# Kernel optimization log

Hardware: AMD Instinct MI355X
Metric: run time of the kernel (lower is better)

Reference implementation:

```python
import jax, jax.numpy as jnp
import numpy as np

B, S, D = 4, 4096, 1024
DFF = 4 * D
ACTIVE = 1024  # ceil(S * 0.25)


def setup_inputs() -> dict:
    key = jax.random.key(0)
    ks = jax.random.split(key, 4)
    x = jax.random.normal(ks[0], (B, S, D), dtype=jnp.float32)
    rw = jax.random.normal(ks[1], (D,), dtype=jnp.float32) * 0.02
    rb = jnp.zeros((1,), dtype=jnp.float32)
    w1 = jax.random.normal(ks[2], (D, DFF), dtype=jnp.float32) * 0.02
    b1 = jnp.zeros((DFF,), dtype=jnp.float32)
    w2 = jax.random.normal(ks[3], (DFF, D), dtype=jnp.float32) * 0.02
    b2 = jnp.zeros((D,), dtype=jnp.float32)
    return {"x": x, "rw": rw, "rb": rb, "w1": w1, "b1": b1,
            "w2": w2, "b2": b2, "active_tokens": ACTIVE}


def reference(x, rw, rb, w1, b1, w2, b2, active_tokens):
    b, s, d = x.shape
    # router: Linear(n_embd, 1) -> [B, S] scores
    scores = jnp.einsum('bsd,d->bs', x, rw) + rb[0]
    # top-k tokens per batch row
    _, idx = jax.lax.top_k(scores, active_tokens)          # [B, K] int32
    sel = jnp.take_along_axis(x, idx[..., None], axis=1)   # [B, K, D]
    # dense MLP on selected tokens (exact GELU as in torch nn.GELU)
    h = jax.nn.gelu(jnp.einsum('bkd,df->bkf', sel, w1) + b1, approximate=False)
    out = jnp.einsum('bkf,fd->bkd', h, w2) + b2            # [B, K, D]
    # sigmoid gate from router scores of selected tokens
    gates = jax.nn.sigmoid(jnp.take_along_axis(scores, idx, axis=1))  # [B, K]
    out = out * gates[..., None]
    # scatter back into zeros at selected positions
    flat_idx = (idx + jnp.arange(b, dtype=idx.dtype)[:, None] * s).reshape(-1)
    flat_out = jnp.zeros((b * s, d), dtype=out.dtype)
    flat_out = flat_out.at[flat_idx].set(out.reshape(-1, d))
    return flat_out.reshape(b, s, d)
```

## Files before the change

### kernel.cpp

```cpp
#include <hip/hip_runtime.h>
#include <hip/hip_bf16.h>
#include <cstdint>
#include <cstddef>

#define Bz 4
#define Sz 4096
#define Dz 1024
#define DFFz 4096
#define KACT 1024

typedef __bf16 bf16;
typedef __attribute__((ext_vector_type(8))) __bf16 bf16x8;
typedef __attribute__((ext_vector_type(4))) __bf16 bf16x4;
typedef __attribute__((ext_vector_type(4))) float f32x4;

__device__ __forceinline__ void async16(const void* g, void* l) {
  __builtin_amdgcn_global_load_lds(
      (const __attribute__((address_space(1))) void*)g,
      (__attribute__((address_space(3))) void*)l, 16, 0, 0);
}

__global__ void router_k(const float* __restrict__ x, const float* __restrict__ rw,
                         const float* __restrict__ rb, float* __restrict__ scores,
                         float4* __restrict__ out4) {
  int row = blockIdx.x * 4 + (threadIdx.x >> 6);
  int lane = threadIdx.x & 63;
  const float4* xr = (const float4*)(x + (size_t)row * Dz);
  const float4* wr = (const float4*)rw;
  float acc = 0.f;
#pragma unroll
  for (int i = 0; i < 4; ++i) {
    float4 a = xr[lane + i * 64];
    float4 w = wr[lane + i * 64];
    acc += a.x * w.x + a.y * w.y + a.z * w.z + a.w * w.w;
  }
#pragma unroll
  for (int d = 32; d; d >>= 1) acc += __shfl_down(acc, d, 64);
  if (lane == 0) scores[row] = acc + rb[0];
  float4* o = out4 + (size_t)blockIdx.x * 4 * (Dz / 4);
  const float4 z = make_float4(0.f, 0.f, 0.f, 0.f);
#pragma unroll
  for (int i = 0; i < 4; ++i) o[threadIdx.x + i * 256] = z;
}

__global__ void transpose_cvt(const float* __restrict__ in, bf16* __restrict__ out,
                              int R, int C) {
  __shared__ float t[32][33];
  int c0 = blockIdx.x * 32, r0 = blockIdx.y * 32;
  int tx = threadIdx.x, ty = threadIdx.y;
#pragma unroll
  for (int i = 0; i < 32; i += 8) t[ty + i][tx] = in[(size_t)(r0 + ty + i) * C + c0 + tx];
  __syncthreads();
#pragma unroll
  for (int i = 0; i < 32; i += 8)
    out[(size_t)(c0 + ty + i) * R + r0 + tx] = (bf16)t[tx][ty + i];
}

__global__ __launch_bounds__(256) void select_gather_k(
    const float* __restrict__ x, const float* __restrict__ scores,
    int* __restrict__ sel_idx, float* __restrict__ gates, bf16* __restrict__ Xsel) {
  int b = blockIdx.x >> 8;
  int s0 = (blockIdx.x & 255) * 16;
  __shared__ float sc[Sz];
  __shared__ int red[16][4];
  __shared__ int rk[16];
  const int tid = threadIdx.x;
  const int wave = tid >> 6, lane = tid & 63;
  const float* srow = scores + (size_t)b * Sz;
#pragma unroll
  for (int i = 0; i < 4; ++i)
    ((float4*)sc)[tid + i * 256] = ((const float4*)srow)[tid + i * 256];
  __syncthreads();
  float mine[16];
#pragma unroll
  for (int j = 0; j < 16; ++j) mine[j] = sc[s0 + j];
  int cnt[16] = {};
  for (int t = tid; t < Sz; t += 256) {
    float o = sc[t];
#pragma unroll
    for (int j = 0; j < 16; ++j)
      cnt[j] += (o > mine[j]) || (o == mine[j] && t < s0 + j);
  }
#pragma unroll
  for (int j = 0; j < 16; ++j) {
    int c = cnt[j];
#pragma unroll
    for (int d = 32; d; d >>= 1) c += __shfl_down(c, d, 64);
    if (lane == 0) red[j][wave] = c;
  }
  __syncthreads();
  if (tid < 16) {
    int rank = red[tid][0] + red[tid][1] + red[tid][2] + red[tid][3];
    rk[tid] = rank;
    if (rank < KACT) {
      int m = b * KACT + rank;
      sel_idx[m] = s0 + tid;
      gates[m] = 1.f / (1.f + expf(-sc[s0 + tid]));
    }
  }
  __syncthreads();
#pragma unroll
  for (int j = 0; j < 16; ++j) {
    int rank = rk[j];
    if (rank >= KACT) continue;
    int m = b * KACT + rank;
    float4 v = ((const float4*)(x + ((size_t)b * Sz + s0 + j) * Dz))[tid];
    bf16x4 o = {(bf16)v.x, (bf16)v.y, (bf16)v.z, (bf16)v.w};
    ((bf16x4*)(Xsel + (size_t)m * Dz))[tid] = o;
  }
}

#define GEMM_BK64_STEP(k0)                                                     \
  _Pragma("unroll")                                                            \
  for (int h = 0; h < 2; ++h) {                                                \
    async16(Ag + (k0) + h * 32, &As[h * 4096 + tid * 8]);                      \
    async16(Ag + (size_t)64 * K + (k0) + h * 32, &As[h * 4096 + 2048 + tid * 8]); \
    async16(Bg + (k0) + h * 32, &Bs[h * 4096 + tid * 8]);                      \
    async16(Bg + (size_t)64 * K + (k0) + h * 32, &Bs[h * 4096 + 2048 + tid * 8]); \
  }                                                                            \
  __syncthreads();                                                             \
  _Pragma("unroll")                                                            \
  for (int h = 0; h < 2; ++h) {                                                \
    bf16x8 af[4], bfr[4];                                                      \
    _Pragma("unroll")                                                          \
    for (int i = 0; i < 4; ++i) {                                              \
      af[i] = *(const bf16x8*)&As[h * 4096 + (wm + i * 16 + l16) * 32 + quad * 8]; \
      bfr[i] = *(const bf16x8*)&Bs[h * 4096 + (wn + i * 16 + l16) * 32 + quad * 8]; \
    }                                                                          \
    _Pragma("unroll")                                                          \
    for (int mi = 0; mi < 4; ++mi)                                             \
      _Pragma("unroll")                                                        \
      for (int ni = 0; ni < 4; ++ni)                                           \
        acc[mi][ni] = __builtin_amdgcn_mfma_f32_16x16x32_bf16(af[mi], bfr[ni], acc[mi][ni], 0, 0, 0); \
  }                                                                            \
  __syncthreads();

__global__ __launch_bounds__(256) void gemm1_k(const bf16* __restrict__ A,
                                               const bf16* __restrict__ Bt,
                                               const float* __restrict__ bias,
                                               bf16* __restrict__ H) {
  constexpr int K = Dz, N = DFFz;
  __shared__ __align__(16) bf16 As[2 * 128 * 32];
  __shared__ __align__(16) bf16 Bs[2 * 128 * 32];
  const int tid = threadIdx.x;
  const int wave = tid >> 6, lane = tid & 63;
  const int quad = lane >> 4, l16 = lane & 15;
  const int m0 = blockIdx.y * 128, n0 = blockIdx.x * 128;
  const int wm = (wave >> 1) * 64, wn = (wave & 1) * 64;
  const int r0 = tid >> 2;
  const int kk = (tid & 3) * 8;
  f32x4 acc[4][4] = {};
  const bf16* Ag = A + (size_t)(m0 + r0) * K + kk;
  const bf16* Bg = Bt + (size_t)(n0 + r0) * K + kk;

  for (int k0 = 0; k0 < K; k0 += 64) {
    GEMM_BK64_STEP(k0)
  }

#pragma unroll
  for (int mi = 0; mi < 4; ++mi) {
    int mbase = m0 + wm + mi * 16 + quad * 4;
#pragma unroll
    for (int ni = 0; ni < 4; ++ni) {
      int n = n0 + wn + ni * 16 + l16;
      float bn = bias[n];
#pragma unroll
      for (int r = 0; r < 4; ++r) {
        float z = acc[mi][ni][r] + bn;
        float g = 0.5f * z * (1.f + erff(z * 0.70710678118654752f));
        H[(size_t)(mbase + r) * N + n] = (bf16)g;
      }
    }
  }
}

__global__ __launch_bounds__(256) void gemm2_k(const bf16* __restrict__ A,
                                               const bf16* __restrict__ Bt,
                                               bf16* __restrict__ P) {
  constexpr int K = DFFz;
  __shared__ __align__(16) bf16 As[2 * 128 * 32];
  __shared__ __align__(16) bf16 Bs[2 * 128 * 32];
  const int tid = threadIdx.x;
  const int wave = tid >> 6, lane = tid & 63;
  const int quad = lane >> 4, l16 = lane & 15;
  const int m0 = blockIdx.y * 128, n0 = blockIdx.x * 128;
  const int kc0 = blockIdx.z * 2048;
  const int wm = (wave >> 1) * 64, wn = (wave & 1) * 64;
  const int r0 = tid >> 2;
  const int kk = (tid & 3) * 8;
  f32x4 acc[4][4] = {};
  const bf16* Ag = A + (size_t)(m0 + r0) * K + kc0 + kk;
  const bf16* Bg = Bt + (size_t)(n0 + r0) * K + kc0 + kk;

  for (int k0 = 0; k0 < 2048; k0 += 64) {
    GEMM_BK64_STEP(k0)
  }

  bf16* Pc = P + (size_t)blockIdx.z * Bz * KACT * Dz;
#pragma unroll
  for (int mi = 0; mi < 4; ++mi) {
    int mbase = m0 + wm + mi * 16 + quad * 4;
#pragma unroll
    for (int ni = 0; ni < 4; ++ni) {
      int n = n0 + wn + ni * 16 + l16;
#pragma unroll
      for (int r = 0; r < 4; ++r)
        Pc[(size_t)(mbase + r) * Dz + n] = (bf16)acc[mi][ni][r];
    }
  }
}

__global__ __launch_bounds__(256) void reduce_k(const bf16* __restrict__ P,
                                                const float* __restrict__ bias,
                                                const int* __restrict__ sel_idx,
                                                const float* __restrict__ gates,
                                                float* __restrict__ out) {
  int m = blockIdx.x;
  int b = m >> 10;
  int s = sel_idx[m];
  float gt = gates[m];
  int tid = threadIdx.x;
  const bf16x4* p0 = (const bf16x4*)(P + (size_t)m * Dz);
  const bf16x4* p1 = (const bf16x4*)(P + (size_t)Bz * KACT * Dz + (size_t)m * Dz);
  const float4* bv = (const float4*)bias;
  float4* orow = (float4*)(out + ((size_t)b * Sz + s) * Dz);
  bf16x4 a = p0[tid], c = p1[tid];
  float4 bb = bv[tid];
  float4 o;
  o.x = ((float)a[0] + (float)c[0] + bb.x) * gt;
  o.y = ((float)a[1] + (float)c[1] + bb.y) * gt;
  o.z = ((float)a[2] + (float)c[2] + bb.z) * gt;
  o.w = ((float)a[3] + (float)c[3] + bb.w) * gt;
  orow[tid] = o;
}

extern "C" void kernel_launch(void* const* d_in, const int* in_sizes, int n_in,
                              void* d_out, int out_size, void* d_ws, size_t ws_size,
                              hipStream_t stream) {
  (void)in_sizes; (void)n_in; (void)out_size; (void)ws_size;
  const float* x  = (const float*)d_in[0];
  const float* rw = (const float*)d_in[1];
  const float* rb = (const float*)d_in[2];
  const float* w1 = (const float*)d_in[3];
  const float* b1 = (const float*)d_in[4];
  const float* w2 = (const float*)d_in[5];
  const float* b2 = (const float*)d_in[6];
  float* out = (float*)d_out;

  char* ws = (char*)d_ws;
  float* scores = (float*)ws;  ws += (size_t)Bz * Sz * 4;
  int*   sel_idx = (int*)ws;   ws += (size_t)Bz * KACT * 4;
  float* gates = (float*)ws;   ws += (size_t)Bz * KACT * 4;
  bf16*  w2T = (bf16*)ws;      ws += (size_t)Dz * DFFz * 2;
  bf16*  H = (bf16*)ws;        ws += (size_t)Bz * KACT * DFFz * 2;
  bf16*  w1T = (bf16*)ws;      ws += (size_t)DFFz * Dz * 2;
  bf16*  Xsel = (bf16*)ws;     ws += (size_t)Bz * KACT * Dz * 2;
  bf16*  P = w1T;

  router_k<<<(Bz * Sz) / 4, 256, 0, stream>>>(x, rw, rb, scores, (float4*)out);
  transpose_cvt<<<dim3(DFFz / 32, Dz / 32), dim3(32, 8), 0, stream>>>(w1, w1T, Dz, DFFz);
  transpose_cvt<<<dim3(Dz / 32, DFFz / 32), dim3(32, 8), 0, stream>>>(w2, w2T, DFFz, Dz);
  select_gather_k<<<Bz * (Sz / 16), 256, 0, stream>>>(x, scores, sel_idx, gates, Xsel);
  gemm1_k<<<dim3(DFFz / 128, (Bz * KACT) / 128), 256, 0, stream>>>(Xsel, w1T, b1, H);
  gemm2_k<<<dim3(Dz / 128, (Bz * KACT) / 128, 2), 256, 0, stream>>>(H, w2T, P);
  reduce_k<<<Bz * KACT, 256, 0, stream>>>(P, b2, sel_idx, gates, out);
}
```

Before: 299.3 us.

## Warp-specialize GEMMs with producer waves and double-buffered LDS

Both GEMM kernels now launch 512 threads: four producer waves issue async global-to-LDS loads for the next K tile into a second LDS buffer while four consumer waves run MFMAs on the current buffer. This is meant to overlap global memory latency with matrix compute, replacing the old load-sync-compute-sync loop. It doubles LDS per block to 64KB and leaves half the waves idle during compute, which may reduce occupancy. The producer waves must still wait on the vmcnt of the async loads before the barrier, otherwise the consumers may read incomplete data.

Measured after the change: 293.0 us. 2.1% less time.

```diff
diff --git a/kernel.cpp b/kernel.cpp
--- a/kernel.cpp
+++ b/kernel.cpp
@@ -110,102 +110,94 @@
   }
 }
 
-#define GEMM_BK64_STEP(k0)                                                     \
+#define PROD_ISSUE(buf, k0)                                                    \
   _Pragma("unroll")                                                            \
   for (int h = 0; h < 2; ++h) {                                                \
-    async16(Ag + (k0) + h * 32, &As[h * 4096 + tid * 8]);                      \
-    async16(Ag + (size_t)64 * K + (k0) + h * 32, &As[h * 4096 + 2048 + tid * 8]); \
-    async16(Bg + (k0) + h * 32, &Bs[h * 4096 + tid * 8]);                      \
-    async16(Bg + (size_t)64 * K + (k0) + h * 32, &Bs[h * 4096 + 2048 + tid * 8]); \
-  }                                                                            \
+    async16(Ag + (k0) + h * 32, &As[buf][h * 4096 + q * 8]);                   \
+    async16(Ag + (size_t)64 * K + (k0) + h * 32, &As[buf][h * 4096 + 2048 + q * 8]); \
+    async16(Bg + (k0) + h * 32, &Bs[buf][h * 4096 + q * 8]);                   \
+    async16(Bg + (size_t)64 * K + (k0) + h * 32, &Bs[buf][h * 4096 + 2048 + q * 8]); \
+  }
+
+#define PIPE_GEMM_BODY(KV, KOFF, NITER)                                        \
+  __shared__ __align__(16) bf16 As[2][2 * 128 * 32];            \
+  __shared__ __align__(16) bf16 Bs[2][2 * 128 * 32];                           \
+  constexpr int K = (KV);                                                      \
+  const int tid = threadIdx.x;                                                 \
+  const int wave = tid >> 6, lane = tid & 63;                                  \
+  const int quad = lane >> 4, l16 = lane & 15;                                 \
+  const int m0 = blockIdx.y * 128, n0 = blockIdx.x * 128;                      \
+  const int wm = (wave >> 1) * 64, wn = (wave & 1) * 64;                       \
+  const int q = tid & 255;                                                     \
+  const bf16* Ag = A + (size_t)(m0 + (q >> 2)) * K + (KOFF) + (q & 3) * 8;     \
+  const bf16* Bg = Bt + (size_t)(n0 + (q >> 2)) * K + (KOFF) + (q & 3) * 8;    \
+  f32x4 acc[4][4] = {};                                                        \
+  if (wave >= 4) { PROD_ISSUE(0, 0) }                                          \
   __syncthreads();                                                             \
-  _Pragma("unroll")                                                            \
-  for (int h = 0; h < 2; ++h) {                                                \
-    bf16x8 af[4], bfr[4];                                                      \
-    _Pragma("unroll")                                                          \
-    for (int i = 0; i < 4; ++i) {                                              \
-      af[i] = *(const bf16x8*)&As[h * 4096 + (wm + i * 16 + l16) * 32 + quad * 8]; \
-      bfr[i] = *(const bf16x8*)&Bs[h * 4096 + (wn + i * 16 + l16) * 32 + quad * 8]; \
+  for (int it = 0; it < (NITER); ++it) {                                       \
+    if (wave >= 4) {                                                           \
+      if (it + 1 < (NITER)) { PROD_ISSUE((it + 1) & 1, (it + 1) * 64) }        \
+    } else {                                                                   \
+      const int cur = it & 1;                                                  \
+      _Pragma("unroll")                                                        \
+      for (int h = 0; h < 2; ++h) {                                            \
+        bf16x8 af[4], bfr[4];                                                  \
+        _Pragma("unroll")                                                      \
+        for (int i = 0; i < 4; ++i) {                                          \
+          af[i] = *(const bf16x8*)&As[cur][h * 4096 + (wm + i * 16 + l16) * 32 + quad * 8]; \
+          bfr[i] = *(const bf16x8*)&Bs[cur][h * 4096 + (wn + i * 16 + l16) * 32 + quad * 8]; \
+        }                                                                      \
+        _Pragma("unroll")                                                      \
+        for (int mi = 0; mi < 4; ++mi)                                         \
+          _Pragma("unroll")                                                    \
+          for (int ni = 0; ni < 4; ++ni)                                       \
+            acc[mi][ni] = __builtin_amdgcn_mfma_f32_16x16x32_bf16(af[mi], bfr[ni], acc[mi][ni], 0, 0, 0); \
+      }                                                                        \
     }                                                                          \
-    _Pragma("unroll")                                                          \
-    for (int mi = 0; mi < 4; ++mi)                                             \
-      _Pragma("unroll")                                                        \
-      for (int ni = 0; ni < 4; ++ni)                                           \
-        acc[mi][ni] = __builtin_amdgcn_mfma_f32_16x16x32_bf16(af[mi], bfr[ni], acc[mi][ni], 0, 0, 0); \
-  }                                                                            \
-  __syncthreads();
-
-__global__ __launch_bounds__(256) void gemm1_k(const bf16* __restrict__ A,
-                                               const bf16* __restrict__ Bt,
-                                               const float* __restrict__ bias,
-                                               bf16* __restrict__ H) {
-  constexpr int K = Dz, N = DFFz;
-  __shared__ __align__(16) bf16 As[2 * 128 * 32];
-  __shared__ __align__(16) bf16 Bs[2 * 128 * 32];
-  const int tid = threadIdx.x;
-  const int wave = tid >> 6, lane = tid & 63;
-  const int quad = lane >> 4, l16 = lane & 15;
-  const int m0 = blockIdx.y * 128, n0 = blockIdx.x * 128;
-  const int wm = (wave >> 1) * 64, wn = (wave & 1) * 64;
-  const int r0 = tid >> 2;
-  const int kk = (tid & 3) * 8;
-  f32x4 acc[4][4] = {};
-  const bf16* Ag = A + (size_t)(m0 + r0) * K + kk;
-  const bf16* Bg = Bt + (size_t)(n0 + r0) * K + kk;
-
-  for (int k0 = 0; k0 < K; k0 += 64) {
-    GEMM_BK64_STEP(k0)
-  }
-
-#pragma unroll
-  for (int mi = 0; mi < 4; ++mi) {
-    int mbase = m0 + wm + mi * 16 + quad * 4;
-#pragma unroll
-    for (int ni = 0; ni < 4; ++ni) {
-      int n = n0 + wn + ni * 16 + l16;
-      float bn = bias[n];
-#pragma unroll
-      for (int r = 0; r < 4; ++r) {
-        float z = acc[mi][ni][r] + bn;
-        float g = 0.5f * z * (1.f + erff(z * 0.70710678118654752f));
-        H[(size_t)(mbase + r) * N + n] = (bf16)g;
+    __syncthreads();                                                           \
+  }
+
+__global__ __launch_bounds__(512, 4) void gemm1_k(const bf16* __restrict__ A,
+                                                  const bf16* __restrict__ Bt,
+                                                  const float* __restrict__ bias,
+                                                  bf16* __restrict__ H) {
+  constexpr int N = DFFz;
+  PIPE_GEMM_BODY(Dz, 0, Dz / 64)
+  if (wave < 4) {
+#pragma unroll
+    for (int mi = 0; mi < 4; ++mi) {
+      int mbase = m0 + wm + mi * 16 + quad * 4;
+#pragma unroll
+      for (int ni = 0; ni < 4; ++ni) {
+        int n = n0 + wn + ni * 16 + l16;
+        float bn = bias[n];
+#pragma unroll
+        for (int r = 0; r < 4; ++r) {
+          float z = acc[mi][ni][r] + bn;
+          float g = 0.5f * z * (1.f + erff(z * 0.70710678118654752f));
+          H[(size_t)(mbase + r) * N + n] = (bf16)g;
+        }
       }
     }
   }
 }
 
-__global__ __launch_bounds__(256) void gemm2_k(const bf16* __restrict__ A,
-                                               const bf16* __restrict__ Bt,
-                                               bf16* __restrict__ P) {
-  constexpr int K = DFFz;
-  __shared__ __align__(16) bf16 As[2 * 128 * 32];
-  __shared__ __align__(16) bf16 Bs[2 * 128 * 32];
-  const int tid = threadIdx.x;
-  const int wave = tid >> 6, lane = tid & 63;
-  const int quad = lane >> 4, l16 = lane & 15;
-  const int m0 = blockIdx.y * 128, n0 = blockIdx.x * 128;
-  const int kc0 = blockIdx.z * 2048;
-  const int wm = (wave >> 1) * 64, wn = (wave & 1) * 64;
-  const int r0 = tid >> 2;
-  const int kk = (tid & 3) * 8;
-  f32x4 acc[4][4] = {};
-  const bf16* Ag = A + (size_t)(m0 + r0) * K + kc0 + kk;
-  const bf16* Bg = Bt + (size_t)(n0 + r0) * K + kc0 + kk;
-
-  for (int k0 = 0; k0 < 2048; k0 += 64) {
-    GEMM_BK64_STEP(k0)
-  }
-
-  bf16* Pc = P + (size_t)blockIdx.z * Bz * KACT * Dz;
-#pragma unroll
-  for (int mi = 0; mi < 4; ++mi) {
-    int mbase = m0 + wm + mi * 16 + quad * 4;
-#pragma unroll
-    for (int ni = 0; ni < 4; ++ni) {
-      int n = n0 + wn + ni * 16 + l16;
-#pragma unroll
-      for (int r = 0; r < 4; ++r)
-        Pc[(size_t)(mbase + r) * Dz + n] = (bf16)acc[mi][ni][r];
+__global__ __launch_bounds__(512, 4) void gemm2_k(const bf16* __restrict__ A,
+                                                  const bf16* __restrict__ Bt,
+                                                  bf16* __restrict__ P) {
+  PIPE_GEMM_BODY(DFFz, blockIdx.z * 2048, 2048 / 64)
+  if (wave < 4) {
+    bf16* Pc = P + (size_t)blockIdx.z * Bz * KACT * Dz;
+#pragma unroll
+    for (int mi = 0; mi < 4; ++mi) {
+      int mbase = m0 + wm + mi * 16 + quad * 4;
+#pragma unroll
+      for (int ni = 0; ni < 4; ++ni) {
+        int n = n0 + wn + ni * 16 + l16;
+#pragma unroll
+        for (int r = 0; r < 4; ++r)
+          Pc[(size_t)(mbase + r) * Dz + n] = (bf16)acc[mi][ni][r];
+      }
     }
   }
 }
@@ -261,7 +253,7 @@
   transpose_cvt<<<dim3(DFFz / 32, Dz / 32), dim3(32, 8), 0, stream>>>(w1, w1T, Dz, DFFz);
   transpose_cvt<<<dim3(Dz / 32, DFFz / 32), dim3(32, 8), 0, stream>>>(w2, w2T, DFFz, Dz);
   select_gather_k<<<Bz * (Sz / 16), 256, 0, stream>>>(x, scores, sel_idx, gates, Xsel);
-  gemm1_k<<<dim3(DFFz / 128, (Bz * KACT) / 128), 256, 0, stream>>>(Xsel, w1T, b1, H);
-  gemm2_k<<<dim3(Dz / 128, (Bz * KACT) / 128, 2), 256, 0, stream>>>(H, w2T, P);
+  gemm1_k<<<dim3(DFFz / 128, (Bz * KACT) / 128), 512, 0, stream>>>(Xsel, w1T, b1, H);
+  gemm2_k<<<dim3(Dz / 128, (Bz * KACT) / 128, 2), 512, 0, stream>>>(H, w2T, P);
   reduce_k<<<Bz * KACT, 256, 0, stream>>>(P, b2, sel_idx, gates, out);
 }
```
